# Kernel optimization log

Hardware: AMD Instinct MI355X
Metric: run time of the kernel (lower is better)

The kernel has to match this reference:

```python
import jax, jax.numpy as jnp
import numpy as np

DIM = 1024

def setup_inputs() -> dict:
    key = jax.random.key(0)
    k1, k2, k3, k4 = jax.random.split(key, 4)
    x = jax.random.normal(k1, (8, 2048, DIM), dtype=jnp.float32)
    # torch Linear weights: y = x @ W.T
    w_qkv = jax.random.normal(k2, (3 * DIM, DIM), dtype=jnp.float32) * (DIM ** -0.5)
    w_proj = jax.random.normal(k3, (DIM, DIM), dtype=jnp.float32) * (DIM ** -0.5)
    b_proj = jax.random.normal(k4, (DIM,), dtype=jnp.float32) * 0.01
    return {"x": x, "w_qkv": w_qkv, "w_proj": w_proj, "b_proj": b_proj}

def reference(x, w_qkv, w_proj, b_proj):
    B, N, C = x.shape
    scale = C ** -0.5
    qkv = jnp.einsum('bnc,dc->bnd', x, w_qkv).reshape(B, N, 3, C)
    q, k, v = qkv[:, :, 0], qkv[:, :, 1], qkv[:, :, 2]  # each [B,N,C]
    attn = jnp.einsum('bnc,bmc->bnm', q, k) * scale      # [B,N,N]
    attn = jax.nn.softmax(attn, axis=-1)
    o = jnp.einsum('bnm,bmc->bnc', attn, v)              # [B,N,C]
    # faithful to torch: (attn@v).transpose(1,2).reshape(B,N,C) permutes data
    o = jnp.swapaxes(o, 1, 2).reshape(B, N, C)
    return jnp.einsum('bnc,dc->bnd', o, w_proj) + b_proj
```

## Files before the change

kernel.cpp:

```cpp
#include <hip/hip_runtime.h>

typedef __bf16 bf16x8_t __attribute__((ext_vector_type(8)));
typedef float f32x4_t __attribute__((ext_vector_type(4)));

#define AS1 __attribute__((address_space(1)))
#define AS3 __attribute__((address_space(3)))

__device__ __forceinline__ unsigned short f2b(float f) {
    unsigned u = __builtin_bit_cast(unsigned, f);
    u += 0x7fffu + ((u >> 16) & 1u);
    return (unsigned short)(u >> 16);
}

__global__ __launch_bounds__(256) void k_f2b(const float* __restrict__ in,
                                             unsigned short* __restrict__ out,
                                             int n4) {
    int i = blockIdx.x * 256 + threadIdx.x;
    if (i >= n4) return;
    float4 v = reinterpret_cast<const float4*>(in)[i];
    ushort4 o;
    o.x = f2b(v.x); o.y = f2b(v.y); o.z = f2b(v.z); o.w = f2b(v.w);
    reinterpret_cast<ushort4*>(out)[i] = o;
}

#define STA(h, i)                                                              \
    __builtin_amdgcn_global_load_lds(                                         \
        (const AS1 void*)(pA + kof + (size_t)((h) * 128 + (i) * 8) * lda),    \
        (AS3 void*)(wb + (h) * 16384 + wave * 2048 + (i) * 1024), 16, 0, 0)
#define STB(h, i)                                                              \
    __builtin_amdgcn_global_load_lds(                                         \
        (const AS1 void*)(pB + kof + (size_t)((h) * 128 + (i) * 8) * ldb),    \
        (AS3 void*)(wb + 32768 + (h) * 16384 + wave * 2048 + (i) * 1024), 16, 0, 0)

#define READ_A(qm)                                                             \
    _Pragma("unroll") for (int mi = 0; mi < 4; ++mi)                           \
        _Pragma("unroll") for (int ks = 0; ks < 2; ++ks)                       \
            af[mi][ks] = *reinterpret_cast<const bf16x8_t*>(rb + offA[qm][mi][ks]);
#define READ_B(qn)                                                             \
    _Pragma("unroll") for (int ni = 0; ni < 2; ++ni)                           \
        _Pragma("unroll") for (int ks = 0; ks < 2; ++ks)                       \
            bf[qn][ni][ks] = *reinterpret_cast<const bf16x8_t*>(rb + offB[qn][ni][ks]);

#define MFMA_QUAD(qm, qn)                                                      \
    __builtin_amdgcn_s_setprio(1);                                             \
    _Pragma("unroll") for (int mi = 0; mi < 4; ++mi)                           \
        _Pragma("unroll") for (int ni = 0; ni < 2; ++ni) {                     \
            acc[qm][qn][mi][ni] = __builtin_amdgcn_mfma_f32_16x16x32_bf16(     \
                af[mi][0], bf[qn][ni][0], acc[qm][qn][mi][ni], 0, 0, 0);       \
            acc[qm][qn][mi][ni] = __builtin_amdgcn_mfma_f32_16x16x32_bf16(     \
                af[mi][1], bf[qn][ni][1], acc[qm][qn][mi][ni], 0, 0, 0);       \
        }                                                                      \
    __builtin_amdgcn_s_setprio(0);

template <bool LAST>
__device__ __forceinline__ void tile_step(
    const char* rb, char* wb, size_t kof,
    const unsigned short* pA, const unsigned short* pB, int lda, int ldb,
    int wave, const int offA[2][4][2], const int offB[2][2][2],
    f32x4_t acc[2][2][4][2]) {
    bf16x8_t af[4][2], bf[2][2][2];
    asm volatile("s_waitcnt vmcnt(2)" ::: "memory");
    asm volatile("s_barrier" ::: "memory");
    if constexpr (!LAST) { STA(0, 0); STA(0, 1); }
    READ_A(0); READ_B(0); READ_B(1);
    MFMA_QUAD(0, 0);
    asm volatile("s_barrier" ::: "memory");
    if constexpr (!LAST) { STB(0, 0); STB(0, 1); }
    MFMA_QUAD(0, 1);
    if constexpr (LAST) asm volatile("s_waitcnt vmcnt(0)" ::: "memory");
    else                asm volatile("s_waitcnt vmcnt(4)" ::: "memory");
    asm volatile("s_barrier" ::: "memory");
    if constexpr (!LAST) { STB(1, 0); STB(1, 1); }
    READ_A(1);
    MFMA_QUAD(1, 1);
    asm volatile("s_barrier" ::: "memory");
    if constexpr (!LAST) { STA(1, 0); STA(1, 1); }
    MFMA_QUAD(1, 0);
}

__device__ __forceinline__ void gemm_mainloop(
    const unsigned short* __restrict__ A, int lda,
    const unsigned short* __restrict__ B, int ldb,
    int K, char* smem, f32x4_t acc[2][2][4][2]) {
    const int tid = threadIdx.x;
    const int wave = tid >> 6, lane = tid & 63;
    const int wsm = (wave >> 2) & 1, wsn = wave & 3;
    const int fr = lane & 15, g = lane >> 4;
    const int srow8 = lane >> 3;
    const int scolB = ((lane & 7) * 16) ^ (srow8 << 4);

    const unsigned short* pA = A + (size_t)(wave * 16 + srow8) * lda + (scolB >> 1);
    const unsigned short* pB = B + (size_t)(wave * 16 + srow8) * ldb + (scolB >> 1);

    int offA[2][4][2], offB[2][2][2];
#pragma unroll
    for (int qm = 0; qm < 2; ++qm)
#pragma unroll
        for (int mi = 0; mi < 4; ++mi)
#pragma unroll
            for (int ks = 0; ks < 2; ++ks)
                offA[qm][mi][ks] = qm * 16384 + (wsm * 64 + mi * 16 + fr) * 128 +
                                   ((ks * 64 + g * 16) ^ ((fr & 7) << 4));
#pragma unroll
    for (int qn = 0; qn < 2; ++qn)
#pragma unroll
        for (int ni = 0; ni < 2; ++ni)
#pragma unroll
            for (int ks = 0; ks < 2; ++ks)
                offB[qn][ni][ks] = 32768 + qn * 16384 + (wsn * 32 + ni * 16 + fr) * 128 +
                                   ((ks * 64 + g * 16) ^ ((fr & 7) << 4));

#pragma unroll
    for (int qm = 0; qm < 2; ++qm)
#pragma unroll
        for (int qn = 0; qn < 2; ++qn)
#pragma unroll
            for (int mi = 0; mi < 4; ++mi)
#pragma unroll
                for (int ni = 0; ni < 2; ++ni)
                    acc[qm][qn][mi][ni] = (f32x4_t){0.f, 0.f, 0.f, 0.f};

    const int NT = K >> 6;

    {
        char* wb = smem;
        const size_t kof = 0;
        STA(0, 0); STA(0, 1);
        STB(0, 0); STB(0, 1);
        STB(1, 0); STB(1, 1);
        STA(1, 0); STA(1, 1);
    }

    for (int t = 0; t < NT - 1; ++t) {
        const char* rb = smem + (size_t)(t & 1) * 65536;
        char* wb = smem + (size_t)((t & 1) ^ 1) * 65536;
        tile_step<false>(rb, wb, (size_t)(t + 1) * 64, pA, pB, lda, ldb,
                         wave, offA, offB, acc);
    }
    {
        const char* rb = smem + (size_t)((NT - 1) & 1) * 65536;
        tile_step<true>(rb, smem, 0, pA, pB, lda, ldb, wave, offA, offB, acc);
    }
}

#define EPILOGUE_IDX                                            \
    const int lane = threadIdx.x & 63, wave = threadIdx.x >> 6; \
    const int e_r0 = ((wave >> 2) & 1) * 64 + (lane >> 4) * 4;  \
    const int e_c0 = (wave & 3) * 32 + (lane & 15);

#define EPILOGUE_LOOP(...)                                      \
    _Pragma("unroll") for (int qm = 0; qm < 2; ++qm)            \
    _Pragma("unroll") for (int qn = 0; qn < 2; ++qn)            \
    _Pragma("unroll") for (int mi = 0; mi < 4; ++mi)            \
    _Pragma("unroll") for (int ni = 0; ni < 2; ++ni)            \
    _Pragma("unroll") for (int j = 0; j < 4; ++j) { __VA_ARGS__ }


__global__ __launch_bounds__(512, 2) void k_gemm_qkv_qk(
    const unsigned short* __restrict__ x, const unsigned short* __restrict__ w,
    unsigned short* __restrict__ qk) {
    __shared__ __align__(16) char smem[131072];
    const size_t tm = (size_t)blockIdx.x * 256, tn = (size_t)blockIdx.y * 256;
    f32x4_t acc[2][2][4][2];
    gemm_mainloop(x + tm * 1024, 1024, w + tn * 1024, 1024, 1024, smem, acc);
    EPILOGUE_IDX
    EPILOGUE_LOOP(
        size_t m = tm + qm * 128 + e_r0 + mi * 16 + j;
        size_t z = m >> 11;
        size_t nloc = m & 2047;
        int n = (int)tn + qn * 128 + e_c0 + ni * 16;
        unsigned short v = f2b(acc[qm][qn][mi][ni][j]);
        size_t base = z * 4194304 + nloc * 1024;
        if (n < 1024) qk[base + n] = v;
        else          qk[base + 2097152 + (n - 1024)] = v;
    )
}

__global__ __launch_bounds__(512, 2) void k_gemm_vt(
    const unsigned short* __restrict__ wv, const unsigned short* __restrict__ x,
    unsigned short* __restrict__ vt) {
    __shared__ __align__(16) char smem[131072];
    const size_t tm = (size_t)blockIdx.x * 256, tn = (size_t)blockIdx.y * 256;
    f32x4_t acc[2][2][4][2];
    gemm_mainloop(wv + tm * 1024, 1024, x + tn * 1024, 1024, 1024, smem, acc);
    EPILOGUE_IDX
    EPILOGUE_LOOP(
        size_t m = tm + qm * 128 + e_r0 + mi * 16 + j;
        size_t n = tn + qn * 128 + e_c0 + ni * 16;
        vt[m * 16384 + n] = f2b(acc[qm][qn][mi][ni][j]);
    )
}

__global__ __launch_bounds__(512, 2) void k_gemm_scores(
    const unsigned short* __restrict__ qk, float* __restrict__ S, int z0) {
    __shared__ __align__(16) char smem[131072];
    const size_t z = z0 + blockIdx.z;
    const size_t tm = (size_t)blockIdx.x * 256, tn = (size_t)blockIdx.y * 256;
    const unsigned short* qz = qk + z * 4194304;
    const unsigned short* kz = qz + 2097152;
    f32x4_t acc[2][2][4][2];
    gemm_mainloop(qz + tm * 1024, 1024, kz + tn * 1024, 1024, 1024, smem, acc);
    EPILOGUE_IDX
    float* Sz = S + (size_t)blockIdx.z * 4194304;
    EPILOGUE_LOOP(
        size_t m = tm + qm * 128 + e_r0 + mi * 16 + j;
        size_t n = tn + qn * 128 + e_c0 + ni * 16;
        Sz[m * 2048 + n] = acc[qm][qn][mi][ni][j] * 0.03125f;
    )
}

__global__ __launch_bounds__(256) void k_softmax(const float* __restrict__ S,
                                                 unsigned short* __restrict__ qk,
                                                 int z0) {
    const size_t r = blockIdx.x;
    const int t = threadIdx.x, wv = t >> 6, ln = t & 63;
    const float4* s4 = reinterpret_cast<const float4*>(S + r * 2048);
    float4 a = s4[t], b = s4[t + 256];
    float vals[8] = {a.x, a.y, a.z, a.w, b.x, b.y, b.z, b.w};

    float mx = vals[0];
#pragma unroll
    for (int i = 1; i < 8; ++i) mx = fmaxf(mx, vals[i]);
#pragma unroll
    for (int i = 32; i > 0; i >>= 1) mx = fmaxf(mx, __shfl_xor(mx, i, 64));
    __shared__ float red[8];
    if (ln == 0) red[wv] = mx;
    __syncthreads();
    mx = fmaxf(fmaxf(red[0], red[1]), fmaxf(red[2], red[3]));

    float ex[8], s = 0.f;
#pragma unroll
    for (int i = 0; i < 8; ++i) { ex[i] = __expf(vals[i] - mx); s += ex[i]; }
#pragma unroll
    for (int i = 32; i > 0; i >>= 1) s += __shfl_xor(s, i, 64);
    if (ln == 0) red[4 + wv] = s;
    __syncthreads();
    s = (red[4] + red[5]) + (red[6] + red[7]);
    float inv = 1.0f / s;

    ushort4 pa, pb;
    pa.x = f2b(ex[0] * inv); pa.y = f2b(ex[1] * inv);
    pa.z = f2b(ex[2] * inv); pa.w = f2b(ex[3] * inv);
    pb.x = f2b(ex[4] * inv); pb.y = f2b(ex[5] * inv);
    pb.z = f2b(ex[6] * inv); pb.w = f2b(ex[7] * inv);

    const size_t zg = z0 + (r >> 11), nloc = r & 2047;
    ushort4* p4 = reinterpret_cast<ushort4*>(qk + zg * 4194304 + nloc * 2048);
    p4[t] = pa;
    p4[t + 256] = pb;
}

__global__ __launch_bounds__(512, 2) void k_gemm_pv(
    const unsigned short* __restrict__ vt, const unsigned short* __restrict__ qk,
    unsigned short* __restrict__ ob, int z0) {
    __shared__ __align__(16) char smem[131072];
    const size_t z = z0 + blockIdx.z;
    const size_t tm = (size_t)blockIdx.x * 256, tn = (size_t)blockIdx.y * 256;
    const unsigned short* P = qk + z * 4194304;
    f32x4_t acc[2][2][4][2];
    gemm_mainloop(vt + tm * 16384 + z * 2048, 16384,
                  P + tn * 2048, 2048, 2048, smem, acc);
    EPILOGUE_IDX
    unsigned short* oz = ob + z * 2097152;
    EPILOGUE_LOOP(
        size_t m = tm + qm * 128 + e_r0 + mi * 16 + j;
        size_t n = tn + qn * 128 + e_c0 + ni * 16;
        oz[(2 * m + (n >> 10)) * 1024 + (n & 1023)] = f2b(acc[qm][qn][mi][ni][j]);
    )
}

__global__ __launch_bounds__(512, 2) void k_gemm_proj(
    const unsigned short* __restrict__ o2, const unsigned short* __restrict__ w,
    const float* __restrict__ bias, float* __restrict__ out) {
    __shared__ __align__(16) char smem[131072];
    const size_t tm = (size_t)blockIdx.x * 256, tn = (size_t)blockIdx.y * 256;
    f32x4_t acc[2][2][4][2];
    gemm_mainloop(o2 + tm * 1024, 1024, w + tn * 1024, 1024, 1024, smem, acc);
    EPILOGUE_IDX
    EPILOGUE_LOOP(
        size_t m = tm + qm * 128 + e_r0 + mi * 16 + j;
        size_t n = tn + qn * 128 + e_c0 + ni * 16;
        out[m * 1024 + n] = acc[qm][qn][mi][ni][j] + bias[n];
    )
}

extern "C" void kernel_launch(void* const* d_in, const int* in_sizes, int n_in,
                              void* d_out, int out_size, void* d_ws, size_t ws_size,
                              hipStream_t stream) {
    const float* x     = (const float*)d_in[0];
    const float* wqkv  = (const float*)d_in[1];
    const float* wproj = (const float*)d_in[2];
    const float* bproj = (const float*)d_in[3];
    float* out = (float*)d_out;
    char* ws = (char*)d_ws;

    const size_t off_xb    = 0;
    const size_t off_wqkv  = 33554432;
    const size_t off_wproj = 39845888;
    const size_t off_qk    = 41943040;
    const size_t off_vt    = 109051904;
    const size_t off_S     = 142606336;
    int NZ = 0;
    for (int c = 8; c >= 1; c >>= 1)
        if (off_S + (size_t)c * 16777216 <= ws_size) { NZ = c; break; }
    if (NZ == 0) return;

    unsigned short* xb     = (unsigned short*)(ws + off_xb);
    unsigned short* wqkvb  = (unsigned short*)(ws + off_wqkv);
    unsigned short* wprojb = (unsigned short*)(ws + off_wproj);
    unsigned short* qkb    = (unsigned short*)(ws + off_qk);
    unsigned short* vtb    = (unsigned short*)(ws + off_vt);
    float*          Sf     = (float*)(ws + off_S);
    unsigned short* obuf   = (unsigned short*)(ws + off_xb);

    k_f2b<<<16384, 256, 0, stream>>>(x, xb, 4194304);
    k_f2b<<<3072, 256, 0, stream>>>(wqkv, wqkvb, 786432);
    k_f2b<<<1024, 256, 0, stream>>>(wproj, wprojb, 262144);

    k_gemm_qkv_qk<<<dim3(64, 8), 512, 0, stream>>>(xb, wqkvb, qkb);
    k_gemm_vt<<<dim3(4, 64), 512, 0, stream>>>(wqkvb + (size_t)2048 * 1024, xb, vtb);

    for (int z0 = 0; z0 < 8; z0 += NZ) {
        k_gemm_scores<<<dim3(8, 8, NZ), 512, 0, stream>>>(qkb, Sf, z0);
        k_softmax<<<NZ * 2048, 256, 0, stream>>>(Sf, qkb, z0);
        k_gemm_pv<<<dim3(4, 8, NZ), 512, 0, stream>>>(vtb, qkb, obuf, z0);
    }
    k_gemm_proj<<<dim3(64, 4), 512, 0, stream>>>(obuf, wprojb, bproj, out);
}
```

Baseline: 373.8 us.

## Restructure GEMM mainloop into 8-phase ping-pong schedule with finer-grained prefetch

Replaces the per-tile step with a two-tile unrolled iteration split into eight phases, each issuing LDS reads and a quarter of the next global-to-LDS loads, then a barrier, waitcnt and an MFMA quad. Loads for subsequent tiles are issued in smaller chunks interleaved across phases, and A/B fragments are reused across adjacent quads to cut LDS reads. The aim is better overlap of memory traffic with MFMA work. In exchange it adds more barriers per tile and assumes NT is even.

```diff
diff --git a/kernel.cpp b/kernel.cpp
--- a/kernel.cpp
+++ b/kernel.cpp
@@ -23,60 +23,84 @@
     reinterpret_cast<ushort4*>(out)[i] = o;
 }
 
-#define STA(h, i)                                                              \
-    __builtin_amdgcn_global_load_lds(                                         \
-        (const AS1 void*)(pA + kof + (size_t)((h) * 128 + (i) * 8) * lda),    \
-        (AS3 void*)(wb + (h) * 16384 + wave * 2048 + (i) * 1024), 16, 0, 0)
-#define STB(h, i)                                                              \
-    __builtin_amdgcn_global_load_lds(                                         \
-        (const AS1 void*)(pB + kof + (size_t)((h) * 128 + (i) * 8) * ldb),    \
-        (AS3 void*)(wb + 32768 + (h) * 16384 + wave * 2048 + (i) * 1024), 16, 0, 0)
-
-#define READ_A(qm)                                                             \
+#define SA(d, h, kof) do {                                                     \
+    char* wb_ = smem + (d) * 65536 + (h) * 16384 + wave * 2048;                \
+    __builtin_amdgcn_global_load_lds(                                          \
+        (const AS1 void*)(pA + (kof) + (size_t)((h) * 128) * lda),             \
+        (AS3 void*)wb_, 16, 0, 0);                                             \
+    __builtin_amdgcn_global_load_lds(                                          \
+        (const AS1 void*)(pA + (kof) + (size_t)((h) * 128 + 8) * lda),         \
+        (AS3 void*)(wb_ + 1024), 16, 0, 0);                                    \
+} while (0)
+#define SB(d, h, kof) do {                                                     \
+    char* wb_ = smem + (d) * 65536 + 32768 + (h) * 16384 + wave * 2048;        \
+    __builtin_amdgcn_global_load_lds(                                          \
+        (const AS1 void*)(pB + (kof) + (size_t)((h) * 128) * ldb),             \
+        (AS3 void*)wb_, 16, 0, 0);                                             \
+    __builtin_amdgcn_global_load_lds(                                          \
+        (const AS1 void*)(pB + (kof) + (size_t)((h) * 128 + 8) * ldb),         \
+        (AS3 void*)(wb_ + 1024), 16, 0, 0);                                    \
+} while (0)
+
+#define RD_A(d, qm, dst)                                                       \
     _Pragma("unroll") for (int mi = 0; mi < 4; ++mi)                           \
-        _Pragma("unroll") for (int ks = 0; ks < 2; ++ks)                       \
-            af[mi][ks] = *reinterpret_cast<const bf16x8_t*>(rb + offA[qm][mi][ks]);
-#define READ_B(qn)                                                             \
+    _Pragma("unroll") for (int ks = 0; ks < 2; ++ks)                           \
+        dst[mi][ks] = *reinterpret_cast<const bf16x8_t*>(                      \
+            smem + (d) * 65536 + offA[qm][mi][ks]);
+#define RD_B(d, qn, dst)                                                       \
     _Pragma("unroll") for (int ni = 0; ni < 2; ++ni)                           \
-        _Pragma("unroll") for (int ks = 0; ks < 2; ++ks)                       \
-            bf[qn][ni][ks] = *reinterpret_cast<const bf16x8_t*>(rb + offB[qn][ni][ks]);
-
-#define MFMA_QUAD(qm, qn)                                                      \
+    _Pragma("unroll") for (int ks = 0; ks < 2; ++ks)                           \
+        dst[ni][ks] = *reinterpret_cast<const bf16x8_t*>(                      \
+            smem + (d) * 65536 + offB[qn][ni][ks]);
+
+#define MFMA_Q(qm, qn, A_, B_)                                                 \
     __builtin_amdgcn_s_setprio(1);                                             \
     _Pragma("unroll") for (int mi = 0; mi < 4; ++mi)                           \
-        _Pragma("unroll") for (int ni = 0; ni < 2; ++ni) {                     \
-            acc[qm][qn][mi][ni] = __builtin_amdgcn_mfma_f32_16x16x32_bf16(     \
-                af[mi][0], bf[qn][ni][0], acc[qm][qn][mi][ni], 0, 0, 0);       \
-            acc[qm][qn][mi][ni] = __builtin_amdgcn_mfma_f32_16x16x32_bf16(     \
-                af[mi][1], bf[qn][ni][1], acc[qm][qn][mi][ni], 0, 0, 0);       \
-        }                                                                      \
-    __builtin_amdgcn_s_setprio(0);
-
-template <bool LAST>
-__device__ __forceinline__ void tile_step(
-    const char* rb, char* wb, size_t kof,
-    const unsigned short* pA, const unsigned short* pB, int lda, int ldb,
-    int wave, const int offA[2][4][2], const int offB[2][2][2],
-    f32x4_t acc[2][2][4][2]) {
-    bf16x8_t af[4][2], bf[2][2][2];
-    asm volatile("s_waitcnt vmcnt(2)" ::: "memory");
-    asm volatile("s_barrier" ::: "memory");
-    if constexpr (!LAST) { STA(0, 0); STA(0, 1); }
-    READ_A(0); READ_B(0); READ_B(1);
-    MFMA_QUAD(0, 0);
-    asm volatile("s_barrier" ::: "memory");
-    if constexpr (!LAST) { STB(0, 0); STB(0, 1); }
-    MFMA_QUAD(0, 1);
-    if constexpr (LAST) asm volatile("s_waitcnt vmcnt(0)" ::: "memory");
-    else                asm volatile("s_waitcnt vmcnt(4)" ::: "memory");
-    asm volatile("s_barrier" ::: "memory");
-    if constexpr (!LAST) { STB(1, 0); STB(1, 1); }
-    READ_A(1);
-    MFMA_QUAD(1, 1);
-    asm volatile("s_barrier" ::: "memory");
-    if constexpr (!LAST) { STA(1, 0); STA(1, 1); }
-    MFMA_QUAD(1, 0);
-}
+    _Pragma("unroll") for (int ni = 0; ni < 2; ++ni) {                         \
+        acc[qm][qn][mi][ni] = __builtin_amdgcn_mfma_f32_16x16x32_bf16(         \
+            A_[mi][0], B_[ni][0], acc[qm][qn][mi][ni], 0, 0, 0);               \
+        acc[qm][qn][mi][ni] = __builtin_amdgcn_mfma_f32_16x16x32_bf16(         \
+            A_[mi][1], B_[ni][1], acc[qm][qn][mi][ni], 0, 0, 0);               \
+    }                                                                          \
+    __builtin_amdgcn_s_setprio(0)
+
+#define PH_SYNC()                                                              \
+    asm volatile("s_barrier" ::: "memory");                                    \
+    asm volatile("s_waitcnt lgkmcnt(0)" ::: "memory");                         \
+    __builtin_amdgcn_sched_barrier(0)
+#define PH_END() asm volatile("s_barrier" ::: "memory")
+
+#define ITER(L, kt1, kt2, kt3) do {                                            \
+    bf16x8_t a_[4][2], b0_[2][2], b1_[2][2];                                   \
+                                                         \
+    RD_A(0, 0, a_); RD_B(0, 0, b0_); SA(1, 1, (kt1));                          \
+    PH_SYNC(); MFMA_Q(0, 0, a_, b0_); PH_END();                                \
+                                                            \
+    RD_B(0, 1, b1_); if (!(L)) SA(0, 0, (kt2));                                \
+    PH_SYNC(); MFMA_Q(0, 1, a_, b1_); PH_END();                                \
+                                                            \
+    RD_A(0, 1, a_); if (!(L)) SB(0, 0, (kt2));                                 \
+    PH_SYNC(); MFMA_Q(1, 1, a_, b1_); PH_END();                                \
+                                                            \
+    if (!(L)) { SB(0, 1, (kt2));                                               \
+                asm volatile("s_waitcnt vmcnt(6)" ::: "memory"); }             \
+    else      { asm volatile("s_waitcnt vmcnt(0)" ::: "memory"); }             \
+    PH_SYNC(); MFMA_Q(1, 0, a_, b0_); PH_END();                                \
+                                                         \
+    RD_A(1, 0, a_); RD_B(1, 0, b0_); if (!(L)) SA(0, 1, (kt2));                \
+    PH_SYNC(); MFMA_Q(0, 0, a_, b0_); PH_END();                                \
+                                                            \
+    RD_B(1, 1, b1_); if (!(L)) SA(1, 0, (kt3));                                \
+    PH_SYNC(); MFMA_Q(0, 1, a_, b1_); PH_END();                                \
+                                                            \
+    RD_A(1, 1, a_); if (!(L)) SB(1, 0, (kt3));                                 \
+    PH_SYNC(); MFMA_Q(1, 1, a_, b1_); PH_END();                                \
+                                                            \
+    if (!(L)) { SB(1, 1, (kt3));                                               \
+                asm volatile("s_waitcnt vmcnt(6)" ::: "memory"); }             \
+    else      { asm volatile("s_waitcnt vmcnt(0)" ::: "memory"); }             \
+    PH_SYNC(); MFMA_Q(1, 0, a_, b0_); PH_END();                                \
+} while (0)
 
 __device__ __forceinline__ void gemm_mainloop(
     const unsigned short* __restrict__ A, int lda,
@@ -121,26 +145,17 @@
                     acc[qm][qn][mi][ni] = (f32x4_t){0.f, 0.f, 0.f, 0.f};
 
     const int NT = K >> 6;
-
-    {
-        char* wb = smem;
-        const size_t kof = 0;
-        STA(0, 0); STA(0, 1);
-        STB(0, 0); STB(0, 1);
-        STB(1, 0); STB(1, 1);
-        STA(1, 0); STA(1, 1);
-    }
-
-    for (int t = 0; t < NT - 1; ++t) {
-        const char* rb = smem + (size_t)(t & 1) * 65536;
-        char* wb = smem + (size_t)((t & 1) ^ 1) * 65536;
-        tile_step<false>(rb, wb, (size_t)(t + 1) * 64, pA, pB, lda, ldb,
-                         wave, offA, offB, acc);
-    }
-    {
-        const char* rb = smem + (size_t)((NT - 1) & 1) * 65536;
-        tile_step<true>(rb, smem, 0, pA, pB, lda, ldb, wave, offA, offB, acc);
-    }
+    const int NI = NT >> 1;
+
+    SA(0, 0, 0); SB(0, 0, 0); SB(0, 1, 0); SA(0, 1, 0);
+    SA(1, 0, 64); SB(1, 0, 64); SB(1, 1, 64);
+    asm volatile("s_waitcnt vmcnt(6)" ::: "memory");
+    asm volatile("s_barrier" ::: "memory");
+
+    size_t kk = 0;
+    for (int i = 0; i < NI - 1; ++i, kk += 128)
+        ITER(0, kk + 64, kk + 128, kk + 192);
+    ITER(1, kk + 64, kk + 128, kk + 192);
 }
 
 #define EPILOGUE_IDX                                            \
```

Measured after the change: 392.8 us. 5.1% more time.

## Store attention scores in bf16 and drop mid-tile barriers in GEMM mainloop

Applied to the files above, without the earlier changes.

The scores GEMM now writes scaled logits as bf16 instead of fp32, and softmax reads them back as bf16. This halves the write and read traffic of the large intermediate score matrix and shrinks its workspace. It costs some precision in the logits before the exponential. In addition, the GEMM tile step issues both the A and B async global-to-LDS loads right after the first barrier of each half and removes two s_barriers per step. That cuts synchronization stalls but risks LDS write/read races if those barriers were protecting buffer reuse.

```diff
diff --git a/kernel.cpp b/kernel.cpp
--- a/kernel.cpp
+++ b/kernel.cpp
@@ -10,6 +10,9 @@
     unsigned u = __builtin_bit_cast(unsigned, f);
     u += 0x7fffu + ((u >> 16) & 1u);
     return (unsigned short)(u >> 16);
+}
+__device__ __forceinline__ float b2f(unsigned short s) {
+    return __builtin_bit_cast(float, (unsigned)s << 16);
 }
 
 __global__ __launch_bounds__(256) void k_f2b(const float* __restrict__ in,
@@ -61,20 +64,16 @@
     bf16x8_t af[4][2], bf[2][2][2];
     asm volatile("s_waitcnt vmcnt(2)" ::: "memory");
     asm volatile("s_barrier" ::: "memory");
-    if constexpr (!LAST) { STA(0, 0); STA(0, 1); }
+    if constexpr (!LAST) { STA(0, 0); STA(0, 1); STB(0, 0); STB(0, 1); }
     READ_A(0); READ_B(0); READ_B(1);
     MFMA_QUAD(0, 0);
-    asm volatile("s_barrier" ::: "memory");
-    if constexpr (!LAST) { STB(0, 0); STB(0, 1); }
     MFMA_QUAD(0, 1);
     if constexpr (LAST) asm volatile("s_waitcnt vmcnt(0)" ::: "memory");
     else                asm volatile("s_waitcnt vmcnt(4)" ::: "memory");
     asm volatile("s_barrier" ::: "memory");
-    if constexpr (!LAST) { STB(1, 0); STB(1, 1); }
+    if constexpr (!LAST) { STB(1, 0); STB(1, 1); STA(1, 0); STA(1, 1); }
     READ_A(1);
     MFMA_QUAD(1, 1);
-    asm volatile("s_barrier" ::: "memory");
-    if constexpr (!LAST) { STA(1, 0); STA(1, 1); }
     MFMA_QUAD(1, 0);
 }
 
@@ -192,7 +191,7 @@
 }
 
 __global__ __launch_bounds__(512, 2) void k_gemm_scores(
-    const unsigned short* __restrict__ qk, float* __restrict__ S, int z0) {
+    const unsigned short* __restrict__ qk, unsigned short* __restrict__ S, int z0) {
     __shared__ __align__(16) char smem[131072];
     const size_t z = z0 + blockIdx.z;
     const size_t tm = (size_t)blockIdx.x * 256, tn = (size_t)blockIdx.y * 256;
@@ -201,22 +200,25 @@
     f32x4_t acc[2][2][4][2];
     gemm_mainloop(qz + tm * 1024, 1024, kz + tn * 1024, 1024, 1024, smem, acc);
     EPILOGUE_IDX
-    float* Sz = S + (size_t)blockIdx.z * 4194304;
+    unsigned short* Sz = S + (size_t)blockIdx.z * 4194304;
     EPILOGUE_LOOP(
         size_t m = tm + qm * 128 + e_r0 + mi * 16 + j;
         size_t n = tn + qn * 128 + e_c0 + ni * 16;
-        Sz[m * 2048 + n] = acc[qm][qn][mi][ni][j] * 0.03125f;
-    )
-}
-
-__global__ __launch_bounds__(256) void k_softmax(const float* __restrict__ S,
+        Sz[m * 2048 + n] = f2b(acc[qm][qn][mi][ni][j] * 0.03125f);
+    )
+}
+
+__global__ __launch_bounds__(256) void k_softmax(const unsigned short* __restrict__ S,
                                                  unsigned short* __restrict__ qk,
                                                  int z0) {
     const size_t r = blockIdx.x;
     const int t = threadIdx.x, wv = t >> 6, ln = t & 63;
-    const float4* s4 = reinterpret_cast<const float4*>(S + r * 2048);
-    float4 a = s4[t], b = s4[t + 256];
-    float vals[8] = {a.x, a.y, a.z, a.w, b.x, b.y, b.z, b.w};
+    const uint4 u = reinterpret_cast<const uint4*>(S + r * 2048)[t];
+    float vals[8];
+    vals[0] = b2f((unsigned short)(u.x & 0xffff)); vals[1] = b2f((unsigned short)(u.x >> 16));
+    vals[2] = b2f((unsigned short)(u.y & 0xffff)); vals[3] = b2f((unsigned short)(u.y >> 16));
+    vals[4] = b2f((unsigned short)(u.z & 0xffff)); vals[5] = b2f((unsigned short)(u.z >> 16));
+    vals[6] = b2f((unsigned short)(u.w & 0xffff)); vals[7] = b2f((unsigned short)(u.w >> 16));
 
     float mx = vals[0];
 #pragma unroll
@@ -238,16 +240,14 @@
     s = (red[4] + red[5]) + (red[6] + red[7]);
     float inv = 1.0f / s;
 
-    ushort4 pa, pb;
-    pa.x = f2b(ex[0] * inv); pa.y = f2b(ex[1] * inv);
-    pa.z = f2b(ex[2] * inv); pa.w = f2b(ex[3] * inv);
-    pb.x = f2b(ex[4] * inv); pb.y = f2b(ex[5] * inv);
-    pb.z = f2b(ex[6] * inv); pb.w = f2b(ex[7] * inv);
+    uint4 o;
+    o.x = (unsigned)f2b(ex[0] * inv) | ((unsigned)f2b(ex[1] * inv) << 16);
+    o.y = (unsigned)f2b(ex[2] * inv) | ((unsigned)f2b(ex[3] * inv) << 16);
+    o.z = (unsigned)f2b(ex[4] * inv) | ((unsigned)f2b(ex[5] * inv) << 16);
+    o.w = (unsigned)f2b(ex[6] * inv) | ((unsigned)f2b(ex[7] * inv) << 16);
 
     const size_t zg = z0 + (r >> 11), nloc = r & 2047;
-    ushort4* p4 = reinterpret_cast<ushort4*>(qk + zg * 4194304 + nloc * 2048);
-    p4[t] = pa;
-    p4[t + 256] = pb;
+    reinterpret_cast<uint4*>(qk + zg * 4194304 + nloc * 2048)[t] = o;
 }
 
 __global__ __launch_bounds__(512, 2) void k_gemm_pv(
@@ -302,7 +302,7 @@
     const size_t off_S     = 142606336;
     int NZ = 0;
     for (int c = 8; c >= 1; c >>= 1)
-        if (off_S + (size_t)c * 16777216 <= ws_size) { NZ = c; break; }
+        if (off_S + (size_t)c * 8388608 <= ws_size) { NZ = c; break; }
     if (NZ == 0) return;
 
     unsigned short* xb     = (unsigned short*)(ws + off_xb);
@@ -310,7 +310,7 @@
     unsigned short* wprojb = (unsigned short*)(ws + off_wproj);
     unsigned short* qkb    = (unsigned short*)(ws + off_qk);
     unsigned short* vtb    = (unsigned short*)(ws + off_vt);
-    float*          Sf     = (float*)(ws + off_S);
+    unsigned short* Sb     = (unsigned short*)(ws + off_S);
     unsigned short* obuf   = (unsigned short*)(ws + off_xb);
 
     k_f2b<<<16384, 256, 0, stream>>>(x, xb, 4194304);
@@ -321,8 +321,8 @@
     k_gemm_vt<<<dim3(4, 64), 512, 0, stream>>>(wqkvb + (size_t)2048 * 1024, xb, vtb);
 
     for (int z0 = 0; z0 < 8; z0 += NZ) {
-        k_gemm_scores<<<dim3(8, 8, NZ), 512, 0, stream>>>(qkb, Sf, z0);
-        k_softmax<<<NZ * 2048, 256, 0, stream>>>(Sf, qkb, z0);
+        k_gemm_scores<<<dim3(8, 8, NZ), 512, 0, stream>>>(qkb, Sb, z0);
+        k_softmax<<<NZ * 2048, 256, 0, stream>>>(Sb, qkb, z0);
         k_gemm_pv<<<dim3(4, 8, NZ), 512, 0, stream>>>(vtb, qkb, obuf, z0);
     }
     k_gemm_proj<<<dim3(64, 4), 512, 0, stream>>>(obuf, wprojb, bproj, out);
```

New measurement: 328.8 us. -12.0%, faster.
